# Optimization experiments

Measured on AMD Instinct MI355X. Metric: run time of the kernel, lower is better.

## Reference

```python
import jax, jax.numpy as jnp
import numpy as np

EPS = 1e-07
NEG = -1e9


def setup_inputs() -> dict:
    key = jax.random.key(0)
    k1, k2, k3, k4 = jax.random.split(key, 4)
    N, M, D = 8192, 8192, 128
    xi = jax.random.normal(k1, (N, D), dtype=jnp.float32)
    xj = jax.random.normal(k2, (M, D), dtype=jnp.float32)
    adj = jax.random.randint(k3, (N, M), 0, 2, dtype=jnp.int32)
    beta = jax.random.uniform(k4, (1,), dtype=jnp.float32)
    return {"xi": xi, "xj": xj, "adj": adj, "beta": beta}


def reference(xi, xj, adj, beta):
    # cosine similarity scores, scaled by learned beta
    xi_norm = jnp.linalg.norm(xi, ord=2, axis=1, keepdims=True)      # [N,1]
    xj_norm = jnp.linalg.norm(xj, ord=2, axis=1, keepdims=True).T    # [1,M]
    cos = beta * (xi @ xj.T) / (xi_norm * xj_norm + EPS)             # [N,M]
    # additive adjacency mask: non-edges pushed to -1e9
    mask = (1.0 - adj.astype(cos.dtype)) * NEG
    P = jax.nn.softmax(cos + mask, axis=1)                           # [N,M]
    return P @ xj                                                    # [N,D]
```

## Files before the change

### kernel.cpp

```cpp
#include <hip/hip_runtime.h>
#include <hip/hip_bf16.h>

typedef float f32x4 __attribute__((ext_vector_type(4)));
typedef short s16x8 __attribute__((ext_vector_type(8)));
typedef unsigned long long ull;

#define NROWS 8192
#define MCOLS 8192
#define DIM   128
#define JSPLIT 8
#define JCHUNK 1024
#define KVB    64
#define ITERS  16

typedef __attribute__((address_space(3))) unsigned int lds_u32;
typedef __attribute__((address_space(1))) unsigned int g_u32;

__device__ __forceinline__ void gl_lds16(const void* g, void* l) {
    __builtin_amdgcn_global_load_lds((const g_u32*)g, (lds_u32*)l, 16, 0, 0);
}

__global__ __launch_bounds__(256) void prep_all(const float* __restrict__ xi,
                                                const float* __restrict__ xj,
                                                const float* __restrict__ beta,
                                                const int* __restrict__ adj,
                                                __hip_bfloat16* __restrict__ Qbf,
                                                __hip_bfloat16* __restrict__ Kbf,
                                                __hip_bfloat16* __restrict__ Vt,
                                                ull* __restrict__ bm) {
    __shared__ float tile[64][65];
    const int tid  = threadIdx.x;
    const int w    = tid >> 6;
    const int lane = tid & 63;

    {
        float b = beta[0];
#pragma unroll
        for (int sub = 0; sub < 2; ++sub) {
            int gr = blockIdx.x * 8 + w * 2 + sub;
            const float* src;
            __hip_bfloat16* dst;
            int row;
            if (gr < NROWS) { row = gr;          src = xi; dst = Qbf; }
            else            { row = gr - NROWS;  src = xj; dst = Kbf; }
            const float* xr = src + (size_t)row * DIM;
            float x0 = xr[lane], x1 = xr[lane + 64];
            float ss = x0 * x0 + x1 * x1;
#pragma unroll
            for (int off = 32; off >= 1; off >>= 1) ss += __shfl_xor(ss, off);
            float s = 1.0f / sqrtf(ss);
            if (gr < NROWS) s *= b;
            __hip_bfloat16* o = dst + (size_t)row * DIM;
            o[lane]      = __float2bfloat16(x0 * s);
            o[lane + 64] = __float2bfloat16(x1 * s);
        }
    }

    if (blockIdx.x < 256) {
        int j0 = (blockIdx.x & 127) * 64;
        int d0 = (blockIdx.x >> 7) * 64;
#pragma unroll
        for (int c = 0; c < 16; ++c) {
            int idx = tid + 256 * c;
            int jr = idx >> 6, dc = idx & 63;
            tile[jr][dc] = xj[(size_t)(j0 + jr) * DIM + d0 + dc];
        }
        __syncthreads();
#pragma unroll
        for (int c = 0; c < 16; ++c) {
            int idx = tid + 256 * c;
            int dr = idx >> 6, jc = idx & 63;
            Vt[(size_t)(d0 + dr) * MCOLS + j0 + jc] = __float2bfloat16(tile[jc][dr]);
        }
        __syncthreads();
    }

    const int gw = (int)((blockIdx.x * 256 + tid) >> 6);
#pragma unroll 2
    for (int s = 0; s < 32; ++s) {
        int win = gw + s * 8192;
        const int* base = adj + (size_t)win * 256;
        int a0 = base[lane], a1 = base[64 + lane], a2 = base[128 + lane], a3 = base[192 + lane];
        ull b0 = __ballot(a0 != 0);
        ull b1 = __ballot(a1 != 0);
        ull b2 = __ballot(a2 != 0);
        ull b3 = __ballot(a3 != 0);
        if (lane < 4) {
            ull v = (lane == 0) ? b0 : ((lane == 1) ? b1 : ((lane == 2) ? b2 : b3));
            bm[(size_t)win * 4 + lane] = v;
        }
    }
}

__global__ __launch_bounds__(256, 2) void flash9(const __hip_bfloat16* __restrict__ Qbf,
                                                 const __hip_bfloat16* __restrict__ Kbf,
                                                 const __hip_bfloat16* __restrict__ Vt,
                                                 const ull* __restrict__ bm,
                                                 float* __restrict__ Opart,
                                                 float* __restrict__ Lpart) {
    __shared__ char smem[74752];
    __hip_bfloat16* Plds = (__hip_bfloat16*)(smem + 65536);

    const int tid  = threadIdx.x;
    const int w    = tid >> 6;
    const int lane = tid & 63;
    const int g    = lane >> 4;
    const int ln   = lane & 15;
    const int bid  = blockIdx.x;
    const int jc   = bid & (JSPLIT - 1);
    const int rt   = bid >> 3;
    const int wrow = rt * 64 + w * 16;
    const int jbase = jc * JCHUNK;

    s16x8 qf[4];
#pragma unroll
    for (int kt = 0; kt < 4; ++kt)
        qf[kt] = *(const s16x8*)(Qbf + (size_t)(wrow + ln) * DIM + kt * 32 + g * 8);

    f32x4 zero = {0.f, 0.f, 0.f, 0.f};
    f32x4 acc[8];
#pragma unroll
    for (int dt = 0; dt < 8; ++dt) acc[dt] = zero;
    float lr[4] = {0.f, 0.f, 0.f, 0.f};

    __hip_bfloat16* pme = Plds + w * (16 * 72);

    auto STAGE = [&](int jt, int b) {
        char* kb = smem + b * 32768;
        char* vb = kb + 16384;
#pragma unroll
        for (int p = 0; p < 4; ++p) {
            int S = p * 256 + tid;
            int row = S >> 4, u = S & 15;
            gl_lds16((const char*)Kbf + (((size_t)(jt + row)) << 8) + ((u ^ (row & 7)) << 4),
                     kb + p * 4096 + w * 1024);
        }
#pragma unroll
        for (int p = 0; p < 4; ++p) {
            int S = p * 256 + tid;
            int row = S >> 3, u = S & 7;
            gl_lds16((const char*)Vt + (((size_t)row) << 14) + (((size_t)jt) << 1) + ((u ^ (row & 7)) << 4),
                     vb + p * 4096 + w * 1024);
        }
    };

    STAGE(jbase, 0);
    __syncthreads();
    int cur = 0;

    for (int it = 0; it < ITERS; ++it) {
        const int jt = jbase + it * KVB;

        ull mw[4];
#pragma unroll
        for (int r = 0; r < 4; ++r)
            mw[r] = bm[(size_t)(wrow + g * 4 + r) * 128 + (jt >> 6)];
        __builtin_amdgcn_sched_barrier(0);

        STAGE(jbase + ((it + 1) & (ITERS - 1)) * KVB, cur ^ 1);

        unsigned short* Klds = (unsigned short*)(smem + cur * 32768);
        unsigned short* Vlds = (unsigned short*)(smem + cur * 32768 + 16384);

        f32x4 s4[4];
#pragma unroll
        for (int ct = 0; ct < 4; ++ct) {
            f32x4 s = zero;
#pragma unroll
            for (int kt = 0; kt < 4; ++kt) {
                int row = ct * 16 + ln;
                s16x8 kf = *(const s16x8*)(Klds + row * 128 + (((kt * 4 + g) ^ (ln & 7)) << 3));
                s = __builtin_amdgcn_mfma_f32_16x16x32_bf16(qf[kt], kf, s, 0, 0, 0);
            }
            s4[ct] = s;
        }

#pragma unroll
        for (int r = 0; r < 4; ++r) {
#pragma unroll
            for (int ct = 0; ct < 4; ++ct) {
                float p = ((mw[r] >> (ct * 16 + ln)) & 1) ? __expf(s4[ct][r]) : 0.f;
                lr[r] += p;
                pme[(g * 4 + r) * 72 + ct * 16 + ln] = __float2bfloat16(p);
            }
        }

#pragma unroll
        for (int kt2 = 0; kt2 < 2; ++kt2) {
            s16x8 pf = *(const s16x8*)(pme + ln * 72 + kt2 * 32 + g * 8);
#pragma unroll
            for (int dt = 0; dt < 8; ++dt) {
                int row = dt * 16 + ln;
                s16x8 vf = *(const s16x8*)(Vlds + row * 64 + (((kt2 * 4 + g) ^ (ln & 7)) << 3));
                acc[dt] = __builtin_amdgcn_mfma_f32_16x16x32_bf16(pf, vf, acc[dt], 0, 0, 0);
            }
        }

        __syncthreads();
        cur ^= 1;
    }

#pragma unroll
    for (int r = 0; r < 4; ++r) {
        lr[r] += __shfl_xor(lr[r], 1);
        lr[r] += __shfl_xor(lr[r], 2);
        lr[r] += __shfl_xor(lr[r], 4);
        lr[r] += __shfl_xor(lr[r], 8);
    }

    float* ob = Opart + ((size_t)jc * NROWS + wrow + g * 4) * DIM;
#pragma unroll
    for (int r = 0; r < 4; ++r)
#pragma unroll
        for (int dt = 0; dt < 8; ++dt)
            ob[(size_t)r * DIM + dt * 16 + ln] = acc[dt][r];
    if (ln == 0) {
#pragma unroll
        for (int r = 0; r < 4; ++r)
            Lpart[(size_t)jc * NROWS + wrow + g * 4 + r] = lr[r];
    }
}

__global__ __launch_bounds__(256) void merge9(const float* __restrict__ Opart,
                                              const float* __restrict__ Lpart,
                                              float* __restrict__ out) {
    int gid = blockIdx.x * 256 + threadIdx.x;
    int row = gid >> 5;
    int dq  = (gid & 31) * 4;
    float4 sum = {0.f, 0.f, 0.f, 0.f};
    float L = 0.f;
#pragma unroll
    for (int jc = 0; jc < JSPLIT; ++jc) {
        float4 v = *(const float4*)(Opart + ((size_t)jc * NROWS + row) * DIM + dq);
        sum.x += v.x; sum.y += v.y; sum.z += v.z; sum.w += v.w;
        L += Lpart[(size_t)jc * NROWS + row];
    }
    float inv = 1.0f / fmaxf(L, 1e-37f);
    float4 ov = {sum.x * inv, sum.y * inv, sum.z * inv, sum.w * inv};
    *(float4*)(out + (size_t)row * DIM + dq) = ov;
}

extern "C" void kernel_launch(void* const* d_in, const int* in_sizes, int n_in,
                              void* d_out, int out_size, void* d_ws, size_t ws_size,
                              hipStream_t stream) {
    const float* xi   = (const float*)d_in[0];
    const float* xj   = (const float*)d_in[1];
    const int*   adj  = (const int*)d_in[2];
    const float* beta = (const float*)d_in[3];
    float* out = (float*)d_out;

    char* ws = (char*)d_ws;
    __hip_bfloat16* Qbf = (__hip_bfloat16*)ws;
    __hip_bfloat16* Kbf = (__hip_bfloat16*)(ws + (size_t)NROWS * DIM * 2);
    __hip_bfloat16* Vt  = (__hip_bfloat16*)(ws + 2 * (size_t)NROWS * DIM * 2);
    ull*            bm  = (ull*)(ws + 3 * (size_t)NROWS * DIM * 2);
    float*          Op  = (float*)(ws + 3 * (size_t)NROWS * DIM * 2 + (size_t)NROWS * (MCOLS / 8));
    float*          Lp  = (float*)((char*)Op + (size_t)JSPLIT * NROWS * DIM * 4);

    hipLaunchKernelGGL(prep_all, dim3(2048), dim3(256), 0, stream, xi, xj, beta, adj, Qbf, Kbf, Vt, bm);
    hipLaunchKernelGGL(flash9, dim3(128 * JSPLIT), dim3(256), 0, stream, Qbf, Kbf, Vt, bm, Op, Lp);
    hipLaunchKernelGGL(merge9, dim3(1024), dim3(256), 0, stream, Op, Lp, out);
}
```

Measured before the change: 127.4 us.

## Process two 16-row query tiles per wave to reuse K/V LDS fragments

Each wave now handles 32 query rows (two 16-row tiles) instead of 16, so every K and V fragment read from LDS feeds two MFMAs. Each block covers 128 rows and the grid is halved to 512 blocks. The P staging buffer moves to an XOR-swizzled layout with no padding, to avoid LDS bank conflicts. This cuts LDS and global K/V traffic per unit of compute, at the cost of twice the accumulator registers and fewer blocks, which may hurt occupancy or CU fill on a 256-CU part.

```diff
diff --git a/kernel.cpp b/kernel.cpp
--- a/kernel.cpp
+++ b/kernel.cpp
@@ -92,14 +92,13 @@
     }
 }
 
-__global__ __launch_bounds__(256, 2) void flash9(const __hip_bfloat16* __restrict__ Qbf,
-                                                 const __hip_bfloat16* __restrict__ Kbf,
-                                                 const __hip_bfloat16* __restrict__ Vt,
-                                                 const ull* __restrict__ bm,
-                                                 float* __restrict__ Opart,
-                                                 float* __restrict__ Lpart) {
-    __shared__ char smem[74752];
-    __hip_bfloat16* Plds = (__hip_bfloat16*)(smem + 65536);
+__global__ __launch_bounds__(256, 2) void flash10(const __hip_bfloat16* __restrict__ Qbf,
+                                                  const __hip_bfloat16* __restrict__ Kbf,
+                                                  const __hip_bfloat16* __restrict__ Vt,
+                                                  const ull* __restrict__ bm,
+                                                  float* __restrict__ Opart,
+                                                  float* __restrict__ Lpart) {
+    __shared__ char smem[81920];
 
     const int tid  = threadIdx.x;
     const int w    = tid >> 6;
@@ -109,25 +108,30 @@
     const int bid  = blockIdx.x;
     const int jc   = bid & (JSPLIT - 1);
     const int rt   = bid >> 3;
-    const int wrow = rt * 64 + w * 16;
+    const int wra  = rt * 128 + w * 32;
     const int jbase = jc * JCHUNK;
-
-    s16x8 qf[4];
-#pragma unroll
-    for (int kt = 0; kt < 4; ++kt)
-        qf[kt] = *(const s16x8*)(Qbf + (size_t)(wrow + ln) * DIM + kt * 32 + g * 8);
+    const int lx   = ln & 7;
+
+    s16x8 qf[2][4];
+#pragma unroll
+    for (int ti = 0; ti < 2; ++ti)
+#pragma unroll
+        for (int kt = 0; kt < 4; ++kt)
+            qf[ti][kt] = *(const s16x8*)(Qbf + (size_t)(wra + ti * 16 + ln) * DIM + kt * 32 + g * 8);
 
     f32x4 zero = {0.f, 0.f, 0.f, 0.f};
-    f32x4 acc[8];
-#pragma unroll
-    for (int dt = 0; dt < 8; ++dt) acc[dt] = zero;
-    float lr[4] = {0.f, 0.f, 0.f, 0.f};
-
-    __hip_bfloat16* pme = Plds + w * (16 * 72);
+    f32x4 acc[2][8];
+#pragma unroll
+    for (int ti = 0; ti < 2; ++ti)
+#pragma unroll
+        for (int dt = 0; dt < 8; ++dt) acc[ti][dt] = zero;
+    float lr[2][4] = {{0.f, 0.f, 0.f, 0.f}, {0.f, 0.f, 0.f, 0.f}};
+
+    char* pw = smem + 65536 + w * 4096;
 
     auto STAGE = [&](int jt, int b) {
-        char* kb = smem + b * 32768;
-        char* vb = kb + 16384;
+        char* kb = smem + b * 16384;
+        char* vb = smem + 32768 + b * 16384;
 #pragma unroll
         for (int p = 0; p < 4; ++p) {
             int S = p * 256 + tid;
@@ -151,48 +155,59 @@
     for (int it = 0; it < ITERS; ++it) {
         const int jt = jbase + it * KVB;
 
-        ull mw[4];
-#pragma unroll
-        for (int r = 0; r < 4; ++r)
-            mw[r] = bm[(size_t)(wrow + g * 4 + r) * 128 + (jt >> 6)];
+        ull mw[2][4];
+#pragma unroll
+        for (int ti = 0; ti < 2; ++ti)
+#pragma unroll
+            for (int r = 0; r < 4; ++r)
+                mw[ti][r] = bm[(size_t)(wra + ti * 16 + g * 4 + r) * 128 + (jt >> 6)];
         __builtin_amdgcn_sched_barrier(0);
 
         STAGE(jbase + ((it + 1) & (ITERS - 1)) * KVB, cur ^ 1);
 
-        unsigned short* Klds = (unsigned short*)(smem + cur * 32768);
-        unsigned short* Vlds = (unsigned short*)(smem + cur * 32768 + 16384);
-
-        f32x4 s4[4];
-#pragma unroll
-        for (int ct = 0; ct < 4; ++ct) {
-            f32x4 s = zero;
+        const char* kb = smem + cur * 16384;
+        const char* vb = smem + 32768 + cur * 16384;
+
+        f32x4 s4[2][4];
+#pragma unroll
+        for (int ti = 0; ti < 2; ++ti)
+#pragma unroll
+            for (int ct = 0; ct < 4; ++ct) s4[ti][ct] = zero;
+#pragma unroll
+        for (int ct = 0; ct < 4; ++ct)
 #pragma unroll
             for (int kt = 0; kt < 4; ++kt) {
-                int row = ct * 16 + ln;
-                s16x8 kf = *(const s16x8*)(Klds + row * 128 + (((kt * 4 + g) ^ (ln & 7)) << 3));
-                s = __builtin_amdgcn_mfma_f32_16x16x32_bf16(qf[kt], kf, s, 0, 0, 0);
+                s16x8 kf = *(const s16x8*)(kb + (ct * 16 + ln) * 256 + (((kt * 4 + g) ^ lx) << 4));
+                s4[0][ct] = __builtin_amdgcn_mfma_f32_16x16x32_bf16(qf[0][kt], kf, s4[0][ct], 0, 0, 0);
+                s4[1][ct] = __builtin_amdgcn_mfma_f32_16x16x32_bf16(qf[1][kt], kf, s4[1][ct], 0, 0, 0);
             }
-            s4[ct] = s;
-        }
-
-#pragma unroll
-        for (int r = 0; r < 4; ++r) {
-#pragma unroll
-            for (int ct = 0; ct < 4; ++ct) {
-                float p = ((mw[r] >> (ct * 16 + ln)) & 1) ? __expf(s4[ct][r]) : 0.f;
-                lr[r] += p;
-                pme[(g * 4 + r) * 72 + ct * 16 + ln] = __float2bfloat16(p);
+
+#pragma unroll
+        for (int ti = 0; ti < 2; ++ti)
+#pragma unroll
+            for (int r = 0; r < 4; ++r) {
+                const int row = g * 4 + r;
+                const int rs = row & 7;
+#pragma unroll
+                for (int ct = 0; ct < 4; ++ct) {
+                    float p = ((mw[ti][r] >> (ct * 16 + ln)) & 1) ? __expf(s4[ti][ct][r]) : 0.f;
+                    lr[ti][r] += p;
+                    *(__hip_bfloat16*)(pw + ti * 2048 + row * 128 +
+                                       (((ct * 2 + (ln >> 3)) ^ rs) << 4) + (ln & 7) * 2)
+                        = __float2bfloat16(p);
+                }
             }
-        }
 
 #pragma unroll
         for (int kt2 = 0; kt2 < 2; ++kt2) {
-            s16x8 pf = *(const s16x8*)(pme + ln * 72 + kt2 * 32 + g * 8);
+            const int uo = ((kt2 * 4 + g) ^ lx) << 4;
+            s16x8 pf0 = *(const s16x8*)(pw + ln * 128 + uo);
+            s16x8 pf1 = *(const s16x8*)(pw + 2048 + ln * 128 + uo);
 #pragma unroll
             for (int dt = 0; dt < 8; ++dt) {
-                int row = dt * 16 + ln;
-                s16x8 vf = *(const s16x8*)(Vlds + row * 64 + (((kt2 * 4 + g) ^ (ln & 7)) << 3));
-                acc[dt] = __builtin_amdgcn_mfma_f32_16x16x32_bf16(pf, vf, acc[dt], 0, 0, 0);
+                s16x8 vf = *(const s16x8*)(vb + (dt * 16 + ln) * 128 + uo);
+                acc[0][dt] = __builtin_amdgcn_mfma_f32_16x16x32_bf16(pf0, vf, acc[0][dt], 0, 0, 0);
+                acc[1][dt] = __builtin_amdgcn_mfma_f32_16x16x32_bf16(pf1, vf, acc[1][dt], 0, 0, 0);
             }
         }
 
@@ -201,29 +216,34 @@
     }
 
 #pragma unroll
-    for (int r = 0; r < 4; ++r) {
-        lr[r] += __shfl_xor(lr[r], 1);
-        lr[r] += __shfl_xor(lr[r], 2);
-        lr[r] += __shfl_xor(lr[r], 4);
-        lr[r] += __shfl_xor(lr[r], 8);
-    }
-
-    float* ob = Opart + ((size_t)jc * NROWS + wrow + g * 4) * DIM;
-#pragma unroll
-    for (int r = 0; r < 4; ++r)
-#pragma unroll
-        for (int dt = 0; dt < 8; ++dt)
-            ob[(size_t)r * DIM + dt * 16 + ln] = acc[dt][r];
-    if (ln == 0) {
+    for (int ti = 0; ti < 2; ++ti)
+#pragma unroll
+        for (int r = 0; r < 4; ++r) {
+            lr[ti][r] += __shfl_xor(lr[ti][r], 1);
+            lr[ti][r] += __shfl_xor(lr[ti][r], 2);
+            lr[ti][r] += __shfl_xor(lr[ti][r], 4);
+            lr[ti][r] += __shfl_xor(lr[ti][r], 8);
+        }
+
+#pragma unroll
+    for (int ti = 0; ti < 2; ++ti) {
+        float* ob = Opart + ((size_t)jc * NROWS + wra + ti * 16 + g * 4) * DIM;
 #pragma unroll
         for (int r = 0; r < 4; ++r)
-            Lpart[(size_t)jc * NROWS + wrow + g * 4 + r] = lr[r];
-    }
-}
-
-__global__ __launch_bounds__(256) void merge9(const float* __restrict__ Opart,
-                                              const float* __restrict__ Lpart,
-                                              float* __restrict__ out) {
+#pragma unroll
+            for (int dt = 0; dt < 8; ++dt)
+                ob[(size_t)r * DIM + dt * 16 + ln] = acc[ti][dt][r];
+        if (ln == 0) {
+#pragma unroll
+            for (int r = 0; r < 4; ++r)
+                Lpart[(size_t)jc * NROWS + wra + ti * 16 + g * 4 + r] = lr[ti][r];
+        }
+    }
+}
+
+__global__ __launch_bounds__(256) void merge10(const float* __restrict__ Opart,
+                                               const float* __restrict__ Lpart,
+                                               float* __restrict__ out) {
     int gid = blockIdx.x * 256 + threadIdx.x;
     int row = gid >> 5;
     int dq  = (gid & 31) * 4;
@@ -258,6 +278,6 @@
     float*          Lp  = (float*)((char*)Op + (size_t)JSPLIT * NROWS * DIM * 4);
 
     hipLaunchKernelGGL(prep_all, dim3(2048), dim3(256), 0, stream, xi, xj, beta, adj, Qbf, Kbf, Vt, bm);
-    hipLaunchKernelGGL(flash9, dim3(128 * JSPLIT), dim3(256), 0, stream, Qbf, Kbf, Vt, bm, Op, Lp);
-    hipLaunchKernelGGL(merge9, dim3(1024), dim3(256), 0, stream, Op, Lp, out);
-}
+    hipLaunchKernelGGL(flash10, dim3(64 * JSPLIT), dim3(256), 0, stream, Qbf, Kbf, Vt, bm, Op, Lp);
+    hipLaunchKernelGGL(merge10, dim3(1024), dim3(256), 0, stream, Op, Lp, out);
+}
```

New measurement: 118.5 us. 1.08x faster.
